# Kernel tuning notes

Measured on AMD Instinct MI355X. Metric: run time of the kernel, lower is better.

Reference implementation:

```python
import jax, jax.numpy as jnp
import numpy as np

DISCOUNT = 0.99
HORIZON = 16


def setup_inputs() -> dict:
    key = jax.random.key(0)
    k1, k2, k3 = jax.random.split(key, 3)
    T, B = 1024, 4096
    rewards = jax.random.normal(k1, (T, B), dtype=jnp.float32)
    values = jax.random.normal(k2, (T, B), dtype=jnp.float32)
    masks = jax.random.uniform(k3, (T, B), dtype=jnp.float32)
    return {"rewards": rewards, "values": values, "masks": masks}


def _n_step_return(rewards, values, masks, gamma, horizon):
    # rewards/values/masks: [T, B]; time_axis == 0
    T = rewards.shape[0]
    rm = rewards * masks  # masked rewards
    # Pad end of time axis with zeros so every window has length `horizon`;
    # out-of-range rewards contribute 0, matching the truncated MC sum.
    pad = jnp.zeros((horizon - 1,) + rm.shape[1:], rm.dtype)
    rm_p = jnp.concatenate([rm, pad], axis=0)  # [T + horizon - 1, B]
    t = jnp.arange(T)
    idx = t[:, None] + jnp.arange(horizon)[None, :]  # [T, horizon]
    windows = rm_p[idx]  # [T, horizon, B]
    disc = jnp.asarray(gamma, rm.dtype) ** jnp.arange(horizon, dtype=rm.dtype)
    g = jnp.einsum('thb,h->tb', windows, disc)  # windowed discounted sums
    # Bootstrap: gamma^{effective_horizon} * V(s_{min(t+horizon-1, T-1)})
    eff_h = (jnp.minimum(t + horizon, T) - t).astype(rm.dtype)  # [T]
    v_idx = jnp.minimum(t + horizon - 1, T - 1)  # [T]
    g = g + (jnp.asarray(gamma, rm.dtype) ** eff_h)[:, None] * values[v_idx]
    return g


def reference(rewards, values, masks):
    return _n_step_return(rewards, values, masks, DISCOUNT, HORIZON)
```

## Files before the change

kernel.cpp:

```cpp
#include <hip/hip_runtime.h>


constexpr int   T_DIM    = 1024;
constexpr int   B_DIM    = 4096;
constexpr int   H        = 16;
constexpr int   COLS     = 64;
constexpr int   ROWS_OUT = 64;
constexpr int   ROWS_LDS = ROWS_OUT + H - 1;
constexpr int   BLOCK    = 512;
constexpr float GAMMA    = 0.99f;

constexpr float gpow_c(int n) {
    float g = 1.0f;
    for (int i = 0; i < n; ++i) g *= GAMMA;
    return g;
}
constexpr float G16 = gpow_c(16);

__global__ __launch_bounds__(BLOCK, 8)
void NStepReturn_88691074662796_kernel(const float* __restrict__ rewards,
                                       const float* __restrict__ values,
                                       const float* __restrict__ masks,
                                       float* __restrict__ out)
{
    __shared__ float rm[ROWS_LDS * COLS];

    const int c0  = blockIdx.x * COLS;
    const int t0  = blockIdx.y * ROWS_OUT;
    const int tid = threadIdx.x;

    const int c     = tid & (COLS - 1);
    const int s     = tid >> 6;
    const int tbase = t0 + s * 8;

    float v[8];
    #pragma unroll
    for (int j = 0; j < 8; ++j) {
        const int vi = min(tbase + j + H - 1, T_DIM - 1);
        v[j] = values[vi * B_DIM + c0 + c];
    }

    #pragma unroll
    for (int base = 0; base < ROWS_LDS * COLS; base += BLOCK) {
        const int j = base + tid;
        if (j < ROWS_LDS * COLS) {
            const int i  = j >> 6;
            const int cc = j & (COLS - 1);
            const int t  = t0 + i;
            float x = 0.0f;
            if (t < T_DIM) {
                x = rewards[t * B_DIM + c0 + cc] * masks[t * B_DIM + c0 + cc];
            }
            rm[j] = x;
        }
    }
    __syncthreads();

    const float* col = &rm[(s * 8) * COLS + c];

    float W = 0.0f;
    #pragma unroll
    for (int h = H - 1; h >= 0; --h) {
        W = col[(7 + h) * COLS] + GAMMA * W;
    }

    {
        const int t = tbase + 7;
        float gb = G16;
        if (t + H > T_DIM) {
            gb = 1.0f;
            for (int k = 0; k < T_DIM - t; ++k) gb *= GAMMA;
        }
        out[t * B_DIM + c0 + c] = W + gb * v[7];
    }

    #pragma unroll
    for (int j = 6; j >= 0; --j) {
        W = col[j * COLS] + GAMMA * W - G16 * col[(j + H) * COLS];

        const int t = tbase + j;
        float gb = G16;
        if (t + H > T_DIM) {
            gb = 1.0f;
            for (int k = 0; k < T_DIM - t; ++k) gb *= GAMMA;
        }
        out[t * B_DIM + c0 + c] = W + gb * v[j];
    }
}

extern "C" void kernel_launch(void* const* d_in, const int* in_sizes, int n_in,
                              void* d_out, int out_size, void* d_ws, size_t ws_size,
                              hipStream_t stream) {
    const float* rewards = (const float*)d_in[0];
    const float* values  = (const float*)d_in[1];
    const float* masks   = (const float*)d_in[2];
    float* out = (float*)d_out;

    dim3 grid(B_DIM / COLS, T_DIM / ROWS_OUT);
    dim3 block(BLOCK);
    NStepReturn_88691074662796_kernel<<<grid, block, 0, stream>>>(rewards, values, masks, out);
}
```

Before: 92.93 us.

## Stage rewards, masks and values into LDS via direct global-to-LDS loads

Replaces the register-staged loads with __builtin_amdgcn_global_load_lds 16-byte transfers that write rewards, masks and values straight into shared memory. The reward-mask product moves into the compute loop. The tile shrinks to 32 output rows with 256 threads, and the occupancy hint is removed. The aim is to cut VGPR traffic and issue wider loads, at the cost of more LDS per block, recomputed products, and more halo overhead (48 rows loaded for 32 outputs).

```diff
diff --git a/kernel.cpp b/kernel.cpp
--- a/kernel.cpp
+++ b/kernel.cpp
@@ -5,9 +5,9 @@
 constexpr int   B_DIM    = 4096;
 constexpr int   H        = 16;
 constexpr int   COLS     = 64;
-constexpr int   ROWS_OUT = 64;
-constexpr int   ROWS_LDS = ROWS_OUT + H - 1;
-constexpr int   BLOCK    = 512;
+constexpr int   ROWS_OUT = 32;
+constexpr int   ROWS_LDS = 48;
+constexpr int   BLOCK    = 256;
 constexpr float GAMMA    = 0.99f;
 
 constexpr float gpow_c(int n) {
@@ -17,74 +17,93 @@
 }
 constexpr float G16 = gpow_c(16);
 
-__global__ __launch_bounds__(BLOCK, 8)
+constexpr int NG_RM = ROWS_LDS / 4;
+constexpr int NG_V  = ROWS_OUT / 4;
+constexpr int NG    = 2 * NG_RM + NG_V;
+
+__device__ __forceinline__ void async_g2l16(const float* gp, float* lds_base) {
+    __builtin_amdgcn_global_load_lds(
+        (const __attribute__((address_space(1))) void*)gp,
+        (__attribute__((address_space(3))) void*)lds_base, 16, 0, 0);
+}
+
+__global__ __launch_bounds__(BLOCK)
 void NStepReturn_88691074662796_kernel(const float* __restrict__ rewards,
                                        const float* __restrict__ values,
                                        const float* __restrict__ masks,
                                        float* __restrict__ out)
 {
-    __shared__ float rm[ROWS_LDS * COLS];
+    __shared__ float lds_r[ROWS_LDS * COLS];
+    __shared__ float lds_m[ROWS_LDS * COLS];
+    __shared__ float lds_v[ROWS_OUT * COLS];
 
-    const int c0  = blockIdx.x * COLS;
-    const int t0  = blockIdx.y * ROWS_OUT;
-    const int tid = threadIdx.x;
+    const int tid  = threadIdx.x;
+    const int c0   = blockIdx.x * COLS;
+    const int t0   = blockIdx.y * ROWS_OUT;
+    const int w    = tid >> 6;
+    const int lane = tid & 63;
+    const int rowsub = lane >> 4;
+    const int colsub = (lane & 15) * 4;
 
-    const int c     = tid & (COLS - 1);
-    const int s     = tid >> 6;
-    const int tbase = t0 + s * 8;
-
-    float v[8];
-    #pragma unroll
-    for (int j = 0; j < 8; ++j) {
-        const int vi = min(tbase + j + H - 1, T_DIM - 1);
-        v[j] = values[vi * B_DIM + c0 + c];
-    }
-
-    #pragma unroll
-    for (int base = 0; base < ROWS_LDS * COLS; base += BLOCK) {
-        const int j = base + tid;
-        if (j < ROWS_LDS * COLS) {
-            const int i  = j >> 6;
-            const int cc = j & (COLS - 1);
-            const int t  = t0 + i;
-            float x = 0.0f;
-            if (t < T_DIM) {
-                x = rewards[t * B_DIM + c0 + cc] * masks[t * B_DIM + c0 + cc];
+    for (int g = w; g < NG; g += 4) {
+        if (g < NG_RM) {
+            const int gi = g;
+            if (t0 + 4 * gi < T_DIM) {
+                const int t = t0 + 4 * gi + rowsub;
+                async_g2l16(rewards + (size_t)t * B_DIM + (c0 + colsub), &lds_r[gi * 256]);
+            } else {
+                *(float4*)&lds_r[gi * 256 + lane * 4] = make_float4(0.f, 0.f, 0.f, 0.f);
             }
-            rm[j] = x;
+        } else if (g < 2 * NG_RM) {
+            const int gi = g - NG_RM;
+            if (t0 + 4 * gi < T_DIM) {
+                const int t = t0 + 4 * gi + rowsub;
+                async_g2l16(masks + (size_t)t * B_DIM + (c0 + colsub), &lds_m[gi * 256]);
+            } else {
+                *(float4*)&lds_m[gi * 256 + lane * 4] = make_float4(0.f, 0.f, 0.f, 0.f);
+            }
+        } else {
+            const int gi  = g - 2 * NG_RM;
+            const int row = 4 * gi + rowsub;
+            const int tv  = min(t0 + H - 1 + row, T_DIM - 1);
+            async_g2l16(values + (size_t)tv * B_DIM + (c0 + colsub), &lds_v[gi * 256]);
         }
     }
     __syncthreads();
 
-    const float* col = &rm[(s * 8) * COLS + c];
+    const int c  = lane;
+    const int r0 = w * 8;
 
     float W = 0.0f;
     #pragma unroll
     for (int h = H - 1; h >= 0; --h) {
-        W = col[(7 + h) * COLS] + GAMMA * W;
+        const int row = r0 + 7 + h;
+        W = lds_r[row * COLS + c] * lds_m[row * COLS + c] + GAMMA * W;
     }
 
     {
-        const int t = tbase + 7;
+        const int t = t0 + r0 + 7;
         float gb = G16;
         if (t + H > T_DIM) {
             gb = 1.0f;
             for (int k = 0; k < T_DIM - t; ++k) gb *= GAMMA;
         }
-        out[t * B_DIM + c0 + c] = W + gb * v[7];
+        out[(size_t)t * B_DIM + c0 + c] = W + gb * lds_v[(r0 + 7) * COLS + c];
     }
 
     #pragma unroll
     for (int j = 6; j >= 0; --j) {
-        W = col[j * COLS] + GAMMA * W - G16 * col[(j + H) * COLS];
+        const int rj = r0 + j;
+        W = lds_r[rj * COLS + c] * lds_m[rj * COLS + c] + GAMMA * W
+          - G16 * lds_r[(rj + H) * COLS + c] * lds_m[(rj + H) * COLS + c];
 
-        const int t = tbase + j;
+        const int t = t0 + rj;
         float gb = G16;
         if (t + H > T_DIM) {
             gb = 1.0f;
             for (int k = 0; k < T_DIM - t; ++k) gb *= GAMMA;
         }
-        out[t * B_DIM + c0 + c] = W + gb * v[j];
+        out[(size_t)t * B_DIM + c0 + c] = W + gb * lds_v[rj * COLS + c];
     }
 }
 
```

Measured after the change: 93.71 us. About the same (+0.8%).
